# Kernel tuning notes

Measured on AMD Instinct MI355X. Metric: run time of the kernel, lower is better.

The kernel has to match this reference:

```python
import jax, jax.numpy as jnp
import numpy as np

WS = 7            # window size (Wh = Ww = 7)
N = WS * WS       # tokens per window = 49
C = 96            # dim
H = 3             # num_heads
HD = C // H       # head_dim = 32
SCALE = HD ** -0.5
B_ = 8192         # num_windows * batch


def _rel_pos_index():
    coords = np.stack(np.meshgrid(np.arange(WS), np.arange(WS), indexing='ij'))  # [2,WS,WS]
    cf = coords.reshape(2, -1)                      # [2,N]
    rel = (cf[:, :, None] - cf[:, None, :]).transpose(1, 2, 0).astype(np.int64)  # [N,N,2]
    rel[:, :, 0] += WS - 1
    rel[:, :, 1] += WS - 1
    rel[:, :, 0] *= 2 * WS - 1
    return rel.sum(-1)                              # [N,N] in [0, 169)

REL_IDX = jnp.asarray(_rel_pos_index())


def _dwconv(img, kern):
    # img: [B,Wh,Ww,C], kern: [3,3,1,C] depthwise
    return jax.lax.conv_general_dilated(
        img, kern, window_strides=(1, 1), padding='SAME',
        dimension_numbers=('NHWC', 'HWIO', 'NHWC'), feature_group_count=C)


def _l2norm(t, eps=1e-12):
    n = jnp.sqrt(jnp.sum(t * t, axis=-1, keepdims=True))
    return t / jnp.maximum(n, eps)


def _forward(x, rpb_table, wq, bq, wk, bk, wv, bv, w_ps, b_ps,
             wq_sp, wk_sp, w_pc, b_pc, conv1, conv2, w_proj, b_proj):
    B = x.shape[0]
    # ---- spatial branch (windowed MHSA with relative position bias) ----
    q = (x @ wq + bq).reshape(B, N, H, HD).transpose(0, 2, 1, 3)  # [B,H,N,HD]
    k = (x @ wk + bk).reshape(B, N, H, HD).transpose(0, 2, 1, 3)
    v_inp = x @ wv + bv                                            # [B,N,C]
    v = v_inp.reshape(B, N, H, HD).transpose(0, 2, 1, 3)
    attn = jnp.einsum('bhnd,bhmd->bhnm', q * SCALE, k)             # [B,H,N,N]
    rpb = rpb_table[REL_IDX.reshape(-1)].reshape(N, N, H).transpose(2, 0, 1)  # [H,N,N]
    attn = jax.nn.softmax(attn + rpb[None], axis=-1)
    sp = jnp.einsum('bhnm,bhmd->bhnd', attn, v).transpose(0, 2, 1, 3).reshape(B, N, C)
    spatial_x = sp @ w_ps + b_ps                                   # [B,N,C]
    # ---- spectral branch (L2-normalized channel attention) ----
    qs = (x @ wq_sp).reshape(B, N, H, HD).transpose(0, 2, 3, 1)    # [B,H,HD,N]
    ks = (x @ wk_sp).reshape(B, N, H, HD).transpose(0, 2, 3, 1)
    vs = v_inp.reshape(B, N, H, HD).transpose(0, 2, 3, 1)
    qs = _l2norm(qs)
    ks = _l2norm(ks)
    cattn = jax.nn.softmax(jnp.einsum('bhdn,bhen->bhde', ks, qs) * SCALE, axis=-1)  # [B,H,HD,HD]
    xc = jnp.einsum('bhde,bhen->bhdn', cattn, vs)                  # [B,H,HD,N]
    xc = xc.transpose(0, 3, 1, 2).reshape(B, N, C)                 # [B,N,C]
    out_c = (xc @ w_pc + b_pc).reshape(B, WS, WS, C)
    # depthwise-conv positional embedding on v_inp
    v_img = v_inp.reshape(B, WS, WS, C)
    out_p = _dwconv(jax.nn.gelu(_dwconv(v_img, conv1), approximate=False), conv2)
    spectral_x = (out_c + out_p).reshape(B, N, C)
    # ---- fuse ----
    return jnp.concatenate([spatial_x, spectral_x], axis=-1) @ w_proj + b_proj


def setup_inputs() -> dict:
    key = jax.random.key(0)
    ks = jax.random.split(key, 18)
    p = lambda i, shape: jax.random.normal(ks[i], shape, dtype=jnp.float32) * 0.02
    return {
        'x': jax.random.normal(ks[0], (B_, N, C), dtype=jnp.float32),
        'rpb_table': p(1, ((2 * WS - 1) ** 2, H)),
        'wq': p(2, (C, C)), 'bq': p(3, (C,)),
        'wk': p(4, (C, C)), 'bk': p(5, (C,)),
        'wv': p(6, (C, C)), 'bv': p(7, (C,)),
        'w_ps': p(8, (C, C)), 'b_ps': p(9, (C,)),
        'wq_sp': p(10, (C, C)), 'wk_sp': p(11, (C, C)),
        'w_pc': p(12, (C, C)), 'b_pc': p(13, (C,)),
        'conv1': p(14, (3, 3, 1, C)), 'conv2': p(15, (3, 3, 1, C)),
        'w_proj': p(16, (2 * C, C)), 'b_proj': p(17, (C,)),
    }


def reference(x, rpb_table, wq, bq, wk, bk, wv, bv, w_ps, b_ps,
              wq_sp, wk_sp, w_pc, b_pc, conv1, conv2, w_proj, b_proj):
    return _forward(x, rpb_table, wq, bq, wk, bk, wv, bv, w_ps, b_ps,
                    wq_sp, wk_sp, w_pc, b_pc, conv1, conv2, w_proj, b_proj)
```

## Files before the change

### kernel.cpp

```cpp
#include <hip/hip_runtime.h>

#define NTOK 49
#define CDIM 96
#define NH   3
#define HD   32

typedef __bf16 bf16x8 __attribute__((ext_vector_type(8)));
typedef float f32x4 __attribute__((ext_vector_type(4)));

__device__ __forceinline__ unsigned short f2bf(float f) {
  union { float f; unsigned u; } v; v.f = f;
  unsigned r = v.u + 0x7FFFu + ((v.u >> 16) & 1u);
  return (unsigned short)(r >> 16);
}
__device__ __forceinline__ float bf2f(unsigned short h) {
  union { unsigned u; float f; } v; v.u = ((unsigned)h) << 16;
  return v.f;
}

__global__ void prep_weights(const float* __restrict__ wq,
                             const float* __restrict__ wk,
                             const float* __restrict__ wv,
                             const float* __restrict__ wq_sp,
                             const float* __restrict__ wk_sp,
                             const float* __restrict__ w_ps,
                             const float* __restrict__ b_ps,
                             const float* __restrict__ w_pc,
                             const float* __restrict__ b_pc,
                             const float* __restrict__ w_proj,
                             const float* __restrict__ b_proj,
                             unsigned short* __restrict__ wsS,
                             float* __restrict__ wsB)
{
  const int g0 = blockIdx.x * blockDim.x + threadIdx.x;
  const int gs = gridDim.x * blockDim.x;
  const int TOT = 73728 + 96;
  for (int idx = g0; idx < TOT; idx += gs) {
    if (idx < 27648) {
      int o = idx / 96, i = idx % 96;
      float v;
      if (o < 96)       v = wq_sp[i*96 + o];
      else if (o < 192) v = wk_sp[i*96 + (o-96)];
      else              v = wv  [i*96 + (o-192)];
      wsS[idx] = f2bf(v);
    } else if (idx < 46080) {
      int j = idx - 27648, o = j / 96, i = j % 96;
      int h = o >> 6, cc = o & 63;
      wsS[idx] = f2bf((cc < 32) ? wq[i*96 + h*32 + cc] : wk[i*96 + h*32 + (cc-32)]);
    } else if (idx < 55296) {
      int j = idx - 46080, o = j / 96, i = j % 96;
      float a = 0.f;
      for (int k = 0; k < 96; ++k) a += w_ps[i*96+k] * w_proj[k*96+o];
      wsS[idx] = f2bf(a);
    } else if (idx < 64512) {
      int j = idx - 55296, o = j / 96, i = j % 96;
      float a = 0.f;
      for (int k = 0; k < 96; ++k) a += w_pc[i*96+k] * w_proj[(96+k)*96+o];
      wsS[idx] = f2bf(a);
    } else if (idx < 73728) {
      int j = idx - 64512, o = j / 96, i = j % 96;
      wsS[idx] = f2bf(w_proj[(96+i)*96 + o]);
    } else {
      int o = idx - 73728;
      float a = b_proj[o];
      for (int k = 0; k < 96; ++k) {
        a += b_ps[k] * w_proj[k*96+o];
        a += b_pc[k] * w_proj[(96+k)*96+o];
      }
      wsB[o] = a;
    }
  }
}

__global__ __launch_bounds__(256, 3) void winattn_mfma3(
    const float* __restrict__ x,
    const float* __restrict__ rpb,
    const float* __restrict__ bq,
    const float* __restrict__ bk,
    const float* __restrict__ bv,
    const float* __restrict__ conv1w,
    const float* __restrict__ conv2w,
    const unsigned short* __restrict__ wcat1,
    const unsigned short* __restrict__ wcat2,
    const unsigned short* __restrict__ w1b,
    const unsigned short* __restrict__ w2b,
    const unsigned short* __restrict__ wpb,
    const float* __restrict__ bias_all,
    float* __restrict__ out)
{
  __shared__ __align__(16) unsigned short sm[26864];
  const int tid = threadIdx.x;
  const int blk = blockIdx.x;
  enum { X_O = 0, V_O = 4704, QS_O = 9408, KS_O = 14216,
         K_O = 19024, SC_O = 23728 };
  const float SCALE = 0.17677669529663687f;

  const int w  = tid >> 6;
  const int l  = tid & 63;
  const int lr = l & 15;
  const int lg = l >> 4;
  float* const rn = (float*)&sm[K_O];

  {
    const float* xg = x + (size_t)blk * 4704;
    for (int i = tid; i < 1176; i += 256) {
      const float4 v = *(const float4*)&xg[i*4];
      union { unsigned short s[4]; uint2 u; } p;
      p.s[0] = f2bf(v.x); p.s[1] = f2bf(v.y); p.s[2] = f2bf(v.z); p.s[3] = f2bf(v.w);
      *(uint2*)&sm[X_O + i*4] = p.u;
    }
  }
  __syncthreads();

  {
    const int xrow = X_O + (16*w + lr)*96 + lg*8;
    const bf16x8 a0 = *(const bf16x8*)&sm[xrow];
    const bf16x8 a1 = *(const bf16x8*)&sm[xrow + 32];
    const bf16x8 a2 = *(const bf16x8*)&sm[xrow + 64];
    for (int t = 0; t < 18; ++t) {
      const int c = 16*t + lr;
      const bf16x8 b0 = *(const bf16x8*)&wcat1[c*96 + lg*8];
      const bf16x8 b1 = *(const bf16x8*)&wcat1[c*96 + 32 + lg*8];
      const bf16x8 b2 = *(const bf16x8*)&wcat1[c*96 + 64 + lg*8];
      f32x4 acc = {0.f, 0.f, 0.f, 0.f};
      acc = __builtin_amdgcn_mfma_f32_16x16x32_bf16(a0, b0, acc, 0, 0, 0);
      acc = __builtin_amdgcn_mfma_f32_16x16x32_bf16(a1, b1, acc, 0, 0, 0);
      acc = __builtin_amdgcn_mfma_f32_16x16x32_bf16(a2, b2, acc, 0, 0, 0);
      int base, col, strd; float bias = 0.f;
      if (t < 6)       { base = QS_O; col = c;       strd = 98; }
      else if (t < 12) { base = KS_O; col = c - 96;  strd = 98; }
      else             { base = V_O;  col = c - 192; strd = 96; bias = bv[c-192]; }
      #pragma unroll
      for (int r = 0; r < 4; ++r) {
        const int tok = 16*w + lg*4 + r;
        if (tok < NTOK) sm[base + tok*strd + col] = f2bf(acc[r] + bias);
      }
    }
  }
  __syncthreads();

  if (tid < 192) {
    const int c    = (tid < 96) ? tid : tid - 96;
    const int base = (tid < 96) ? QS_O : KS_O;
    float ss = 0.f;
    for (int n = 0; n < NTOK; ++n) { const float v = bf2f(sm[base + n*98 + c]); ss += v*v; }
    rn[tid] = 1.0f / fmaxf(sqrtf(ss), 1e-12f);
  }
  __syncthreads();

  {
    for (int jb = 0; jb < 3; ++jb) {
      const int job = w*3 + jb, rt = job >> 1, ct = job & 1, h = rt >> 1;
      const int qc = h*32 + 16*ct + lr;
      union { unsigned short u[8]; bf16x8 v; } a0u, a1u, b0u, b1u;
      #pragma unroll
      for (int j = 0; j < 8; ++j) {
        const int k0 = lg*8 + j, k1 = 32 + k0;
        a0u.u[j] = sm[KS_O + k0*98 + 16*rt + lr];
        b0u.u[j] = sm[QS_O + k0*98 + qc];
        a1u.u[j] = (k1 < NTOK) ? sm[KS_O + k1*98 + 16*rt + lr] : (unsigned short)0;
        b1u.u[j] = (k1 < NTOK) ? sm[QS_O + k1*98 + qc] : (unsigned short)0;
      }
      f32x4 acc = {0.f, 0.f, 0.f, 0.f};
      acc = __builtin_amdgcn_mfma_f32_16x16x32_bf16(a0u.v, b0u.v, acc, 0, 0, 0);
      acc = __builtin_amdgcn_mfma_f32_16x16x32_bf16(a1u.v, b1u.v, acc, 0, 0, 0);
      const float rq = rn[qc];
      #pragma unroll
      for (int r = 0; r < 4; ++r) {
        const int dq = 16*rt + lg*4 + r;
        sm[SC_O + dq*32 + 16*ct + lr] = f2bf(acc[r] * rq * rn[96 + dq] * SCALE);
      }
    }
  }
  __syncthreads();

  {
    const int xrow = X_O + (16*w + lr)*96 + lg*8;
    const bf16x8 a0 = *(const bf16x8*)&sm[xrow];
    const bf16x8 a1 = *(const bf16x8*)&sm[xrow + 32];
    const bf16x8 a2 = *(const bf16x8*)&sm[xrow + 64];
    for (int t = 0; t < 12; ++t) {
      const int c = 16*t + lr;
      const bf16x8 b0 = *(const bf16x8*)&wcat2[c*96 + lg*8];
      const bf16x8 b1 = *(const bf16x8*)&wcat2[c*96 + 32 + lg*8];
      const bf16x8 b2 = *(const bf16x8*)&wcat2[c*96 + 64 + lg*8];
      f32x4 acc = {0.f, 0.f, 0.f, 0.f};
      acc = __builtin_amdgcn_mfma_f32_16x16x32_bf16(a0, b0, acc, 0, 0, 0);
      acc = __builtin_amdgcn_mfma_f32_16x16x32_bf16(a1, b1, acc, 0, 0, 0);
      acc = __builtin_amdgcn_mfma_f32_16x16x32_bf16(a2, b2, acc, 0, 0, 0);
      const int h = t >> 2;
      const bool isq = (t & 3) < 2;
      const int cc = (t & 1)*16 + lr;
      const float bias = isq ? bq[h*32 + cc] : bk[h*32 + cc];
      const int dst = (isq ? X_O : K_O) + h*32 + cc;
      #pragma unroll
      for (int r = 0; r < 4; ++r) {
        const int tok = 16*w + lg*4 + r;
        if (tok < NTOK) sm[dst + tok*96] = f2bf(acc[r] + bias);
      }
    }
  }
  if (tid < 96) {
    const int base = SC_O + tid*32;
    const int off = (tid * 5) & 31;
    float m = -1e30f;
    for (int jj = 0; jj < 32; ++jj) { const int j = (jj + off) & 31;
      m = fmaxf(m, bf2f(sm[base + j])); }
    float s = 0.f;
    for (int jj = 0; jj < 32; ++jj) { const int j = (jj + off) & 31;
      s += __expf(bf2f(sm[base + j]) - m); }
    const float inv = 1.0f / s;
    for (int jj = 0; jj < 32; ++jj) { const int j = (jj + off) & 31;
      sm[base + j] = f2bf(__expf(bf2f(sm[base + j]) - m) * inv); }
  }
  __syncthreads();

  {
    for (int ctile = 0; ctile < 6; ++ctile) {
      const int h = ctile >> 1;
      const bf16x8 av  = *(const bf16x8*)&sm[V_O + (16*w + lr)*96 + h*32 + lg*8];
      const bf16x8 bc  = *(const bf16x8*)&sm[SC_O + (16*ctile + lr)*32 + lg*8];
      f32x4 acc = {0.f, 0.f, 0.f, 0.f};
      acc = __builtin_amdgcn_mfma_f32_16x16x32_bf16(av, bc, acc, 0, 0, 0);
      #pragma unroll
      for (int r = 0; r < 4; ++r) {
        const int tok = 16*w + lg*4 + r;
        if (tok < NTOK) sm[QS_O + tok*96 + 16*ctile + lr] = f2bf(acc[r]);
      }
    }
  }
  for (int idx = tid; idx < 588; idx += 256) {
    const int n = idx / 12, c0 = (idx % 12) * 8;
    const int y = n / 7, xx = n % 7;
    float a[8];
    #pragma unroll
    for (int j = 0; j < 8; ++j) a[j] = 0.f;
    #pragma unroll
    for (int dy = -1; dy <= 1; ++dy) {
      const int yy = y + dy;
      if (yy < 0 || yy >= 7) continue;
      #pragma unroll
      for (int dx = -1; dx <= 1; ++dx) {
        const int x2 = xx + dx;
        if (x2 < 0 || x2 >= 7) continue;
        union { bf16x8 v; unsigned short u[8]; } iv;
        iv.v = *(const bf16x8*)&sm[V_O + (yy*7 + x2)*96 + c0];
        const float* wp = conv1w + ((dy+1)*3 + (dx+1))*96 + c0;
        #pragma unroll
        for (int j = 0; j < 8; ++j) a[j] += bf2f(iv.u[j]) * wp[j];
      }
    }
    union { unsigned short u[8]; bf16x8 v; } ov;
    #pragma unroll
    for (int j = 0; j < 8; ++j) {
      const float g = a[j];
      ov.u[j] = f2bf(0.5f * g * (1.0f + erff(g * 0.70710678118654752f)));
    }
    *(bf16x8*)&sm[KS_O + n*96 + c0] = ov.v;
  }
  __syncthreads();

  float hov[3][8];
  {
    #pragma unroll
    for (int it = 0; it < 3; ++it) {
      const int e = tid + it*256;
      #pragma unroll
      for (int j = 0; j < 8; ++j) hov[it][j] = 0.f;
      if (e < 588) {
        const int n = e / 12, c0 = (e % 12) * 8;
        const int y = n / 7, xx = n % 7;
        #pragma unroll
        for (int dy = -1; dy <= 1; ++dy) {
          const int yy = y + dy;
          if (yy < 0 || yy >= 7) continue;
          #pragma unroll
          for (int dx = -1; dx <= 1; ++dx) {
            const int x2 = xx + dx;
            if (x2 < 0 || x2 >= 7) continue;
            union { bf16x8 v; unsigned short u[8]; } iv;
            iv.v = *(const bf16x8*)&sm[KS_O + (yy*7 + x2)*96 + c0];
            const float* wp = conv2w + ((dy+1)*3 + (dx+1))*96 + c0;
            #pragma unroll
            for (int j = 0; j < 8; ++j) hov[it][j] += bf2f(iv.u[j]) * wp[j];
          }
        }
      }
    }
    for (int zi = tid; zi < 735; zi += 256)
      sm[SC_O + (zi/15)*64 + 49 + zi%15] = 0;
  }
  __syncthreads();
  {
    #pragma unroll
    for (int it = 0; it < 3; ++it) {
      const int e = tid + it*256;
      if (e < 588) {
        const int n = e / 12, c0 = (e % 12) * 8;
        union { unsigned short u[8]; bf16x8 v; } ov;
        #pragma unroll
        for (int j = 0; j < 8; ++j) ov.u[j] = f2bf(hov[it][j]);
        *(bf16x8*)&sm[KS_O + n*96 + c0] = ov.v;
      }
    }
  }
  __syncthreads();

  for (int h = 0; h < NH; ++h) {
    {
      const bf16x8 aq = *(const bf16x8*)&sm[X_O + (16*w + lr)*96 + h*32 + lg*8];
      #pragma unroll
      for (int nt = 0; nt < 4; ++nt) {
        const bf16x8 bk8 = *(const bf16x8*)&sm[K_O + (16*nt + lr)*96 + h*32 + lg*8];
        f32x4 acc = {0.f, 0.f, 0.f, 0.f};
        acc = __builtin_amdgcn_mfma_f32_16x16x32_bf16(aq, bk8, acc, 0, 0, 0);
        #pragma unroll
        for (int r = 0; r < 4; ++r) {
          const int row = 16*w + lg*4 + r;
          const int col = 16*nt + lr;
          if (row < NTOK && col < NTOK) {
            const int ridx = (row/7 - col/7 + 6)*13 + (row%7 - col%7 + 6);
            sm[SC_O + row*64 + col] = f2bf(acc[r] * SCALE + rpb[ridx*NH + h]);
          }
        }
      }
    }
    __syncthreads();
    if (tid < 196) {
      const int row = tid >> 2, p = tid & 3;
      const int cS = p * 13;
      const int cnt = (p == 3) ? 10 : 13;
      const int ro = row % cnt;
      const int base = SC_O + row*64 + cS;
      float m = -1e30f;
      for (int i = 0; i < cnt; ++i) {
        int j = i + ro; if (j >= cnt) j -= cnt;
        m = fmaxf(m, bf2f(sm[base + j]));
      }
      m = fmaxf(m, __shfl_xor(m, 1, 4));
      m = fmaxf(m, __shfl_xor(m, 2, 4));
      float s = 0.f;
      for (int i = 0; i < cnt; ++i) {
        int j = i + ro; if (j >= cnt) j -= cnt;
        s += __expf(bf2f(sm[base + j]) - m);
      }
      s += __shfl_xor(s, 1, 4);
      s += __shfl_xor(s, 2, 4);
      const float inv = 1.0f / s;
      for (int i = 0; i < cnt; ++i) {
        int j = i + ro; if (j >= cnt) j -= cnt;
        sm[base + j] = f2bf(__expf(bf2f(sm[base + j]) - m) * inv);
      }
    }
    __syncthreads();
    {
      const int prow = (16*w + lr < 48) ? (16*w + lr) : 48;
      const bf16x8 ap0 = *(const bf16x8*)&sm[SC_O + prow*64 + lg*8];
      const bf16x8 ap1 = *(const bf16x8*)&sm[SC_O + prow*64 + 32 + lg*8];
      #pragma unroll
      for (int nt = 0; nt < 2; ++nt) {
        f32x4 acc = {0.f, 0.f, 0.f, 0.f};
        union { unsigned short u[8]; bf16x8 v; } cv;
        #pragma unroll
        for (int j = 0; j < 8; ++j)
          cv.u[j] = sm[V_O + (lg*8 + j)*96 + h*32 + 16*nt + lr];
        acc = __builtin_amdgcn_mfma_f32_16x16x32_bf16(ap0, cv.v, acc, 0, 0, 0);
        #pragma unroll
        for (int j = 0; j < 8; ++j)
          cv.u[j] = sm[V_O + (32 + lg*8 + j)*96 + h*32 + 16*nt + lr];
        acc = __builtin_amdgcn_mfma_f32_16x16x32_bf16(ap1, cv.v, acc, 0, 0, 0);
        #pragma unroll
        for (int r = 0; r < 4; ++r) {
          const int tok = 16*w + lg*4 + r;
          if (tok < NTOK) sm[X_O + tok*96 + h*32 + 16*nt + lr] = f2bf(acc[r]);
        }
      }
    }
    __syncthreads();
  }

  {
    f32x4 acc[6];
    #pragma unroll
    for (int t = 0; t < 6; ++t) acc[t] = (f32x4){0.f, 0.f, 0.f, 0.f};
    const int Ao[3] = { X_O, QS_O, KS_O };
    const unsigned short* const Ws[3] = { w1b, w2b, wpb };
    #pragma unroll
    for (int s = 0; s < 3; ++s) {
      const int arow = Ao[s] + (16*w + lr)*96 + lg*8;
      const bf16x8 a0 = *(const bf16x8*)&sm[arow];
      const bf16x8 a1 = *(const bf16x8*)&sm[arow + 32];
      const bf16x8 a2 = *(const bf16x8*)&sm[arow + 64];
      #pragma unroll
      for (int t = 0; t < 6; ++t) {
        const int o = 16*t + lr;
        const bf16x8 b0 = *(const bf16x8*)&Ws[s][o*96 + lg*8];
        const bf16x8 b1 = *(const bf16x8*)&Ws[s][o*96 + 32 + lg*8];
        const bf16x8 b2 = *(const bf16x8*)&Ws[s][o*96 + 64 + lg*8];
        acc[t] = __builtin_amdgcn_mfma_f32_16x16x32_bf16(a0, b0, acc[t], 0, 0, 0);
        acc[t] = __builtin_amdgcn_mfma_f32_16x16x32_bf16(a1, b1, acc[t], 0, 0, 0);
        acc[t] = __builtin_amdgcn_mfma_f32_16x16x32_bf16(a2, b2, acc[t], 0, 0, 0);
      }
    }
    float* og = out + (size_t)blk * 4704;
    #pragma unroll
    for (int t = 0; t < 6; ++t) {
      const int co = 16*t + lr;
      const float bb = bias_all[co];
      #pragma unroll
      for (int r = 0; r < 4; ++r) {
        const int tok = 16*w + lg*4 + r;
        if (tok < NTOK) og[tok*96 + co] = acc[t][r] + bb;
      }
    }
  }
}

extern "C" void kernel_launch(void* const* d_in, const int* in_sizes, int n_in,
                              void* d_out, int out_size, void* d_ws, size_t ws_size,
                              hipStream_t stream)
{
  const float* x      = (const float*)d_in[0];
  const float* rpbt   = (const float*)d_in[1];
  const float* wq     = (const float*)d_in[2];
  const float* bq     = (const float*)d_in[3];
  const float* wk     = (const float*)d_in[4];
  const float* bk     = (const float*)d_in[5];
  const float* wv     = (const float*)d_in[6];
  const float* bv     = (const float*)d_in[7];
  const float* w_ps   = (const float*)d_in[8];
  const float* b_ps   = (const float*)d_in[9];
  const float* wq_sp  = (const float*)d_in[10];
  const float* wk_sp  = (const float*)d_in[11];
  const float* w_pc   = (const float*)d_in[12];
  const float* b_pc   = (const float*)d_in[13];
  const float* conv1  = (const float*)d_in[14];
  const float* conv2  = (const float*)d_in[15];
  const float* w_proj = (const float*)d_in[16];
  const float* b_proj = (const float*)d_in[17];

  unsigned short* wsS = (unsigned short*)d_ws;
  float* wsB = (float*)((char*)d_ws + (size_t)2*73728);

  prep_weights<<<80, 256, 0, stream>>>(wq, wk, wv, wq_sp, wk_sp, w_ps, b_ps,
                                       w_pc, b_pc, w_proj, b_proj, wsS, wsB);

  const int nblk = in_sizes[0] / (NTOK*CDIM);
  winattn_mfma3<<<nblk, 256, 0, stream>>>(x, rpbt, bq, bk, bv, conv1, conv2,
      wsS, wsS + 27648, wsS + 46080, wsS + 55296, wsS + 64512, wsB,
      (float*)d_out);
}
```

Measured before the change: 871.3 us.

## Merge projection GEMMs, transpose spectral Q/K, precompute RPB, double-buffer head scores

Merges the two input projection MFMA loops into a single 30-tile pass, removing one barrier. Spectral Q/K are stored transposed with vectorized L2 normalization applied in place. The relative position bias is expanded once into a padded table in the prep kernel, and f2bf now uses a native bf16 cast. Per-head attention alternates between two score buffers so one head's PV overlaps the next head's QK^T, which cuts barriers but adds LDS use and layout complexity.

```diff
diff --git a/kernel.cpp b/kernel.cpp
--- a/kernel.cpp
+++ b/kernel.cpp
@@ -4,18 +4,17 @@
 #define CDIM 96
 #define NH   3
 #define HD   32
+#define TS   52
 
 typedef __bf16 bf16x8 __attribute__((ext_vector_type(8)));
 typedef float f32x4 __attribute__((ext_vector_type(4)));
-
-__device__ __forceinline__ unsigned short f2bf(float f) {
-  union { float f; unsigned u; } v; v.f = f;
-  unsigned r = v.u + 0x7FFFu + ((v.u >> 16) & 1u);
-  return (unsigned short)(r >> 16);
+typedef unsigned short u16;
+
+__device__ __forceinline__ u16 f2bf(float f) {
+  union { __bf16 h; u16 u; } v; v.h = (__bf16)f; return v.u;
 }
-__device__ __forceinline__ float bf2f(unsigned short h) {
-  union { unsigned u; float f; } v; v.u = ((unsigned)h) << 16;
-  return v.f;
+__device__ __forceinline__ float bf2f(u16 h) {
+  union { unsigned u; float f; } v; v.u = ((unsigned)h) << 16; return v.f;
 }
 
 __global__ void prep_weights(const float* __restrict__ wq,
@@ -29,12 +28,13 @@
                              const float* __restrict__ b_pc,
                              const float* __restrict__ w_proj,
                              const float* __restrict__ b_proj,
+                             const float* __restrict__ rpb,
                              unsigned short* __restrict__ wsS,
                              float* __restrict__ wsB)
 {
   const int g0 = blockIdx.x * blockDim.x + threadIdx.x;
   const int gs = gridDim.x * blockDim.x;
-  const int TOT = 73728 + 96;
+  const int TOT = 73728 + 96 + 3*49*64;
   for (int idx = g0; idx < TOT; idx += gs) {
     if (idx < 27648) {
       int o = idx / 96, i = idx % 96;
@@ -60,7 +60,7 @@
     } else if (idx < 73728) {
       int j = idx - 64512, o = j / 96, i = j % 96;
       wsS[idx] = f2bf(w_proj[(96+i)*96 + o]);
-    } else {
+    } else if (idx < 73824) {
       int o = idx - 73728;
       float a = b_proj[o];
       for (int k = 0; k < 96; ++k) {
@@ -68,13 +68,21 @@
         a += b_pc[k] * w_proj[(96+k)*96+o];
       }
       wsB[o] = a;
+    } else {
+      int j = idx - 73824;
+      int h = j / 3136, rr = (j % 3136) / 64, cc = j % 64;
+      float v = 0.f;
+      if (cc < NTOK) {
+        const int ridx = (rr/7 - cc/7 + 6)*13 + (rr%7 - cc%7 + 6);
+        v = rpb[ridx*NH + h];
+      }
+      wsB[96 + j] = v;
     }
   }
 }
 
-__global__ __launch_bounds__(256, 3) void winattn_mfma3(
+__global__ __launch_bounds__(256, 3) void winattn_v4(
     const float* __restrict__ x,
-    const float* __restrict__ rpb,
     const float* __restrict__ bq,
     const float* __restrict__ bk,
     const float* __restrict__ bv,
@@ -86,26 +94,26 @@
     const unsigned short* __restrict__ w2b,
     const unsigned short* __restrict__ wpb,
     const float* __restrict__ bias_all,
+    const float* __restrict__ rpbf,
     float* __restrict__ out)
 {
-  __shared__ __align__(16) unsigned short sm[26864];
+  __shared__ __align__(16) u16 sm[27232];
   const int tid = threadIdx.x;
   const int blk = blockIdx.x;
-  enum { X_O = 0, V_O = 4704, QS_O = 9408, KS_O = 14216,
-         K_O = 19024, SC_O = 23728 };
+  enum { X_O = 0, V_O = 4704, QT_O = 9408, KT_O = 14400,
+         K_O = 19392, SC_O = 24096 };
   const float SCALE = 0.17677669529663687f;
 
   const int w  = tid >> 6;
   const int l  = tid & 63;
   const int lr = l & 15;
   const int lg = l >> 4;
-  float* const rn = (float*)&sm[K_O];
 
   {
     const float* xg = x + (size_t)blk * 4704;
     for (int i = tid; i < 1176; i += 256) {
       const float4 v = *(const float4*)&xg[i*4];
-      union { unsigned short s[4]; uint2 u; } p;
+      union { u16 s[4]; uint2 u; } p;
       p.s[0] = f2bf(v.x); p.s[1] = f2bf(v.y); p.s[2] = f2bf(v.z); p.s[3] = f2bf(v.w);
       *(uint2*)&sm[X_O + i*4] = p.u;
     }
@@ -117,89 +125,105 @@
     const bf16x8 a0 = *(const bf16x8*)&sm[xrow];
     const bf16x8 a1 = *(const bf16x8*)&sm[xrow + 32];
     const bf16x8 a2 = *(const bf16x8*)&sm[xrow + 64];
-    for (int t = 0; t < 18; ++t) {
-      const int c = 16*t + lr;
-      const bf16x8 b0 = *(const bf16x8*)&wcat1[c*96 + lg*8];
-      const bf16x8 b1 = *(const bf16x8*)&wcat1[c*96 + 32 + lg*8];
-      const bf16x8 b2 = *(const bf16x8*)&wcat1[c*96 + 64 + lg*8];
+    const int t0 = 16*w + 4*lg;
+    for (int t = 0; t < 30; ++t) {
+      const u16* wsrc = (t < 18) ? &wcat1[(16*t + lr)*96]
+                                 : &wcat2[(16*(t-18) + lr)*96];
+      const bf16x8 b0 = *(const bf16x8*)&wsrc[lg*8];
+      const bf16x8 b1 = *(const bf16x8*)&wsrc[32 + lg*8];
+      const bf16x8 b2 = *(const bf16x8*)&wsrc[64 + lg*8];
       f32x4 acc = {0.f, 0.f, 0.f, 0.f};
       acc = __builtin_amdgcn_mfma_f32_16x16x32_bf16(a0, b0, acc, 0, 0, 0);
       acc = __builtin_amdgcn_mfma_f32_16x16x32_bf16(a1, b1, acc, 0, 0, 0);
       acc = __builtin_amdgcn_mfma_f32_16x16x32_bf16(a2, b2, acc, 0, 0, 0);
-      int base, col, strd; float bias = 0.f;
-      if (t < 6)       { base = QS_O; col = c;       strd = 98; }
-      else if (t < 12) { base = KS_O; col = c - 96;  strd = 98; }
-      else             { base = V_O;  col = c - 192; strd = 96; bias = bv[c-192]; }
-      #pragma unroll
-      for (int r = 0; r < 4; ++r) {
-        const int tok = 16*w + lg*4 + r;
-        if (tok < NTOK) sm[base + tok*strd + col] = f2bf(acc[r] + bias);
+      if (t < 12) {
+        const int base = (t < 6) ? (QT_O + (16*t + lr)*TS)
+                                 : (KT_O + (16*(t-6) + lr)*TS);
+        u16 s0 = f2bf(acc[0]), s1 = f2bf(acc[1]), s2 = f2bf(acc[2]), s3 = f2bf(acc[3]);
+        if (t0 <= 44) {
+          uint2 pk; pk.x = (unsigned)s0 | ((unsigned)s1 << 16);
+          pk.y = (unsigned)s2 | ((unsigned)s3 << 16);
+          *(uint2*)&sm[base + t0] = pk;
+        } else if (t0 == 48) {
+          uint2 pk; pk.x = (unsigned)s0; pk.y = 0u;
+          *(uint2*)&sm[base + 48] = pk;
+        }
+      } else if (t < 18) {
+        const int c = 16*t + lr - 192;
+        const float bias = bv[c];
+        #pragma unroll
+        for (int r = 0; r < 4; ++r) {
+          const int tok = t0 + r;
+          if (tok < NTOK) sm[V_O + tok*96 + c] = f2bf(acc[r] + bias);
+        }
+      } else {
+        const int u = t - 18, h = u >> 2;
+        const bool isq = (u & 3) < 2;
+        const int cc = (u & 1)*16 + lr;
+        const float bias = isq ? bq[h*32 + cc] : bk[h*32 + cc];
+        const int dst = (isq ? X_O : K_O) + h*32 + cc;
+        #pragma unroll
+        for (int r = 0; r < 4; ++r) {
+          const int tok = t0 + r;
+          if (tok < NTOK) sm[dst + tok*96] = f2bf(acc[r] + bias);
+        }
       }
     }
   }
   __syncthreads();
 
   if (tid < 192) {
-    const int c    = (tid < 96) ? tid : tid - 96;
-    const int base = (tid < 96) ? QS_O : KS_O;
+    const int base = (tid < 96) ? (QT_O + tid*TS) : (KT_O + (tid-96)*TS);
     float ss = 0.f;
-    for (int n = 0; n < NTOK; ++n) { const float v = bf2f(sm[base + n*98 + c]); ss += v*v; }
-    rn[tid] = 1.0f / fmaxf(sqrtf(ss), 1e-12f);
+    #pragma unroll
+    for (int i = 0; i < 12; ++i) {
+      const uint2 uu = *(const uint2*)&sm[base + i*4];
+      const float v0 = bf2f((u16)(uu.x & 0xFFFF)), v1 = bf2f((u16)(uu.x >> 16));
+      const float v2 = bf2f((u16)(uu.y & 0xFFFF)), v3 = bf2f((u16)(uu.y >> 16));
+      ss += v0*v0 + v1*v1 + v2*v2 + v3*v3;
+    }
+    { const float v = bf2f(sm[base + 48]); ss += v*v; }
+    const float rn = 1.0f / fmaxf(sqrtf(ss), 1e-12f);
+    #pragma unroll
+    for (int i = 0; i < 12; ++i) {
+      uint2 uu = *(const uint2*)&sm[base + i*4];
+      const u16 o0 = f2bf(bf2f((u16)(uu.x & 0xFFFF)) * rn);
+      const u16 o1 = f2bf(bf2f((u16)(uu.x >> 16)) * rn);
+      const u16 o2 = f2bf(bf2f((u16)(uu.y & 0xFFFF)) * rn);
+      const u16 o3 = f2bf(bf2f((u16)(uu.y >> 16)) * rn);
+      uu.x = (unsigned)o0 | ((unsigned)o1 << 16);
+      uu.y = (unsigned)o2 | ((unsigned)o3 << 16);
+      *(uint2*)&sm[base + i*4] = uu;
+    }
+    sm[base + 48] = f2bf(bf2f(sm[base + 48]) * rn);
   }
   __syncthreads();
 
   {
+    union U8 { uint2 q[2]; bf16x8 v; };
     for (int jb = 0; jb < 3; ++jb) {
       const int job = w*3 + jb, rt = job >> 1, ct = job & 1, h = rt >> 1;
-      const int qc = h*32 + 16*ct + lr;
-      union { unsigned short u[8]; bf16x8 v; } a0u, a1u, b0u, b1u;
-      #pragma unroll
-      for (int j = 0; j < 8; ++j) {
-        const int k0 = lg*8 + j, k1 = 32 + k0;
-        a0u.u[j] = sm[KS_O + k0*98 + 16*rt + lr];
-        b0u.u[j] = sm[QS_O + k0*98 + qc];
-        a1u.u[j] = (k1 < NTOK) ? sm[KS_O + k1*98 + 16*rt + lr] : (unsigned short)0;
-        b1u.u[j] = (k1 < NTOK) ? sm[QS_O + k1*98 + qc] : (unsigned short)0;
-      }
+      const int abase = KT_O + (16*rt + lr)*TS + lg*8;
+      const int bbase = QT_O + (h*32 + 16*ct + lr)*TS + lg*8;
+      U8 A0, B0, A1, B1;
+      A0.q[0] = *(const uint2*)&sm[abase];      A0.q[1] = *(const uint2*)&sm[abase + 4];
+      B0.q[0] = *(const uint2*)&sm[bbase];      B0.q[1] = *(const uint2*)&sm[bbase + 4];
+      A1.q[0] = *(const uint2*)&sm[abase + 32]; A1.q[1] = *(const uint2*)&sm[abase + 36];
+      B1.q[0] = *(const uint2*)&sm[bbase + 32]; B1.q[1] = *(const uint2*)&sm[bbase + 36];
+      if (lg == 2)      { A1.q[0].x &= 0xFFFFu; A1.q[0].y = 0u; A1.q[1].x = 0u; A1.q[1].y = 0u; }
+      else if (lg == 3) { A1.q[0].x = 0u; A1.q[0].y = 0u; A1.q[1].x = 0u; A1.q[1].y = 0u; }
       f32x4 acc = {0.f, 0.f, 0.f, 0.f};
-      acc = __builtin_amdgcn_mfma_f32_16x16x32_bf16(a0u.v, b0u.v, acc, 0, 0, 0);
-      acc = __builtin_amdgcn_mfma_f32_16x16x32_bf16(a1u.v, b1u.v, acc, 0, 0, 0);
-      const float rq = rn[qc];
+      acc = __builtin_amdgcn_mfma_f32_16x16x32_bf16(A0.v, B0.v, acc, 0, 0, 0);
+      acc = __builtin_amdgcn_mfma_f32_16x16x32_bf16(A1.v, B1.v, acc, 0, 0, 0);
       #pragma unroll
       for (int r = 0; r < 4; ++r) {
         const int dq = 16*rt + lg*4 + r;
-        sm[SC_O + dq*32 + 16*ct + lr] = f2bf(acc[r] * rq * rn[96 + dq] * SCALE);
-      }
-    }
-  }
-  __syncthreads();
-
-  {
-    const int xrow = X_O + (16*w + lr)*96 + lg*8;
-    const bf16x8 a0 = *(const bf16x8*)&sm[xrow];
-    const bf16x8 a1 = *(const bf16x8*)&sm[xrow + 32];
-    const bf16x8 a2 = *(const bf16x8*)&sm[xrow + 64];
-    for (int t = 0; t < 12; ++t) {
-      const int c = 16*t + lr;
-      const bf16x8 b0 = *(const bf16x8*)&wcat2[c*96 + lg*8];
-      const bf16x8 b1 = *(const bf16x8*)&wcat2[c*96 + 32 + lg*8];
-      const bf16x8 b2 = *(const bf16x8*)&wcat2[c*96 + 64 + lg*8];
-      f32x4 acc = {0.f, 0.f, 0.f, 0.f};
-      acc = __builtin_amdgcn_mfma_f32_16x16x32_bf16(a0, b0, acc, 0, 0, 0);
-      acc = __builtin_amdgcn_mfma_f32_16x16x32_bf16(a1, b1, acc, 0, 0, 0);
-      acc = __builtin_amdgcn_mfma_f32_16x16x32_bf16(a2, b2, acc, 0, 0, 0);
-      const int h = t >> 2;
-      const bool isq = (t & 3) < 2;
-      const int cc = (t & 1)*16 + lr;
-      const float bias = isq ? bq[h*32 + cc] : bk[h*32 + cc];
-      const int dst = (isq ? X_O : K_O) + h*32 + cc;
-      #pragma unroll
-      for (int r = 0; r < 4; ++r) {
-        const int tok = 16*w + lg*4 + r;
-        if (tok < NTOK) sm[dst + tok*96] = f2bf(acc[r] + bias);
-      }
-    }
-  }
+        sm[SC_O + dq*32 + 16*ct + lr] = f2bf(acc[r] * SCALE);
+      }
+    }
+  }
+  __syncthreads();
+
   if (tid < 96) {
     const int base = SC_O + tid*32;
     const int off = (tid * 5) & 31;
@@ -213,125 +237,35 @@
     for (int jj = 0; jj < 32; ++jj) { const int j = (jj + off) & 31;
       sm[base + j] = f2bf(__expf(bf2f(sm[base + j]) - m) * inv); }
   }
-  __syncthreads();
-
-  {
-    for (int ctile = 0; ctile < 6; ++ctile) {
-      const int h = ctile >> 1;
-      const bf16x8 av  = *(const bf16x8*)&sm[V_O + (16*w + lr)*96 + h*32 + lg*8];
-      const bf16x8 bc  = *(const bf16x8*)&sm[SC_O + (16*ctile + lr)*32 + lg*8];
+  for (int zi = tid; zi < 735; zi += 256)
+    sm[KT_O + (zi/15)*64 + 49 + zi%15] = 0;
+  __syncthreads();
+
+  auto QKT = [&](int h, int scb) {
+    const bf16x8 aq = *(const bf16x8*)&sm[X_O + (16*w + lr)*96 + h*32 + lg*8];
+    #pragma unroll
+    for (int nt = 0; nt < 4; ++nt) {
+      const bf16x8 bk8 = *(const bf16x8*)&sm[K_O + (16*nt + lr)*96 + h*32 + lg*8];
       f32x4 acc = {0.f, 0.f, 0.f, 0.f};
-      acc = __builtin_amdgcn_mfma_f32_16x16x32_bf16(av, bc, acc, 0, 0, 0);
+      acc = __builtin_amdgcn_mfma_f32_16x16x32_bf16(aq, bk8, acc, 0, 0, 0);
+      const int col = 16*nt + lr;
       #pragma unroll
       for (int r = 0; r < 4; ++r) {
-        const int tok = 16*w + lg*4 + r;
-        if (tok < NTOK) sm[QS_O + tok*96 + 16*ctile + lr] = f2bf(acc[r]);
-      }
-    }
-  }
-  for (int idx = tid; idx < 588; idx += 256) {
-    const int n = idx / 12, c0 = (idx % 12) * 8;
-    const int y = n / 7, xx = n % 7;
-    float a[8];
-    #pragma unroll
-    for (int j = 0; j < 8; ++j) a[j] = 0.f;
-    #pragma unroll
-    for (int dy = -1; dy <= 1; ++dy) {
-      const int yy = y + dy;
-      if (yy < 0 || yy >= 7) continue;
-      #pragma unroll
-      for (int dx = -1; dx <= 1; ++dx) {
-        const int x2 = xx + dx;
-        if (x2 < 0 || x2 >= 7) continue;
-        union { bf16x8 v; unsigned short u[8]; } iv;
-        iv.v = *(const bf16x8*)&sm[V_O + (yy*7 + x2)*96 + c0];
-        const float* wp = conv1w + ((dy+1)*3 + (dx+1))*96 + c0;
-        #pragma unroll
-        for (int j = 0; j < 8; ++j) a[j] += bf2f(iv.u[j]) * wp[j];
-      }
-    }
-    union { unsigned short u[8]; bf16x8 v; } ov;
-    #pragma unroll
-    for (int j = 0; j < 8; ++j) {
-      const float g = a[j];
-      ov.u[j] = f2bf(0.5f * g * (1.0f + erff(g * 0.70710678118654752f)));
-    }
-    *(bf16x8*)&sm[KS_O + n*96 + c0] = ov.v;
-  }
-  __syncthreads();
-
-  float hov[3][8];
-  {
-    #pragma unroll
-    for (int it = 0; it < 3; ++it) {
-      const int e = tid + it*256;
-      #pragma unroll
-      for (int j = 0; j < 8; ++j) hov[it][j] = 0.f;
-      if (e < 588) {
-        const int n = e / 12, c0 = (e % 12) * 8;
-        const int y = n / 7, xx = n % 7;
-        #pragma unroll
-        for (int dy = -1; dy <= 1; ++dy) {
-          const int yy = y + dy;
-          if (yy < 0 || yy >= 7) continue;
-          #pragma unroll
-          for (int dx = -1; dx <= 1; ++dx) {
-            const int x2 = xx + dx;
-            if (x2 < 0 || x2 >= 7) continue;
-            union { bf16x8 v; unsigned short u[8]; } iv;
-            iv.v = *(const bf16x8*)&sm[KS_O + (yy*7 + x2)*96 + c0];
-            const float* wp = conv2w + ((dy+1)*3 + (dx+1))*96 + c0;
-            #pragma unroll
-            for (int j = 0; j < 8; ++j) hov[it][j] += bf2f(iv.u[j]) * wp[j];
-          }
-        }
-      }
-    }
-    for (int zi = tid; zi < 735; zi += 256)
-      sm[SC_O + (zi/15)*64 + 49 + zi%15] = 0;
-  }
-  __syncthreads();
-  {
-    #pragma unroll
-    for (int it = 0; it < 3; ++it) {
-      const int e = tid + it*256;
-      if (e < 588) {
-        const int n = e / 12, c0 = (e % 12) * 8;
-        union { unsigned short u[8]; bf16x8 v; } ov;
-        #pragma unroll
-        for (int j = 0; j < 8; ++j) ov.u[j] = f2bf(hov[it][j]);
-        *(bf16x8*)&sm[KS_O + n*96 + c0] = ov.v;
-      }
-    }
-  }
-  __syncthreads();
-
-  for (int h = 0; h < NH; ++h) {
-    {
-      const bf16x8 aq = *(const bf16x8*)&sm[X_O + (16*w + lr)*96 + h*32 + lg*8];
-      #pragma unroll
-      for (int nt = 0; nt < 4; ++nt) {
-        const bf16x8 bk8 = *(const bf16x8*)&sm[K_O + (16*nt + lr)*96 + h*32 + lg*8];
-        f32x4 acc = {0.f, 0.f, 0.f, 0.f};
-        acc = __builtin_amdgcn_mfma_f32_16x16x32_bf16(aq, bk8, acc, 0, 0, 0);
-        #pragma unroll
-        for (int r = 0; r < 4; ++r) {
-          const int row = 16*w + lg*4 + r;
-          const int col = 16*nt + lr;
-          if (row < NTOK && col < NTOK) {
-            const int ridx = (row/7 - col/7 + 6)*13 + (row%7 - col%7 + 6);
-            sm[SC_O + row*64 + col] = f2bf(acc[r] * SCALE + rpb[ridx*NH + h]);
-          }
-        }
-      }
-    }
-    __syncthreads();
+        const int row = 16*w + lg*4 + r;
+        const int rc = (row < 48) ? row : 48;
+        const float bias = rpbf[(h*49 + rc)*64 + col];
+        if (row < NTOK && col < NTOK)
+          sm[scb + row*64 + col] = f2bf(acc[r] * SCALE + bias);
+      }
+    }
+  };
+  auto SMAX = [&](int scb) {
     if (tid < 196) {
       const int row = tid >> 2, p = tid & 3;
       const int cS = p * 13;
       const int cnt = (p == 3) ? 10 : 13;
       const int ro = row % cnt;
-      const int base = SC_O + row*64 + cS;
+      const int base = scb + row*64 + cS;
       float m = -1e30f;
       for (int i = 0; i < cnt; ++i) {
         int j = i + ro; if (j >= cnt) j -= cnt;
@@ -352,39 +286,131 @@
         sm[base + j] = f2bf(__expf(bf2f(sm[base + j]) - m) * inv);
       }
     }
-    __syncthreads();
-    {
-      const int prow = (16*w + lr < 48) ? (16*w + lr) : 48;
-      const bf16x8 ap0 = *(const bf16x8*)&sm[SC_O + prow*64 + lg*8];
-      const bf16x8 ap1 = *(const bf16x8*)&sm[SC_O + prow*64 + 32 + lg*8];
-      #pragma unroll
-      for (int nt = 0; nt < 2; ++nt) {
-        f32x4 acc = {0.f, 0.f, 0.f, 0.f};
-        union { unsigned short u[8]; bf16x8 v; } cv;
+  };
+  auto PV = [&](int h, int scb) {
+    const int prow = (16*w + lr < 48) ? (16*w + lr) : 48;
+    const bf16x8 ap0 = *(const bf16x8*)&sm[scb + prow*64 + lg*8];
+    const bf16x8 ap1 = *(const bf16x8*)&sm[scb + prow*64 + 32 + lg*8];
+    #pragma unroll
+    for (int nt = 0; nt < 2; ++nt) {
+      f32x4 acc = {0.f, 0.f, 0.f, 0.f};
+      union { u16 u[8]; bf16x8 v; } cv;
+      #pragma unroll
+      for (int j = 0; j < 8; ++j)
+        cv.u[j] = sm[V_O + (lg*8 + j)*96 + h*32 + 16*nt + lr];
+      acc = __builtin_amdgcn_mfma_f32_16x16x32_bf16(ap0, cv.v, acc, 0, 0, 0);
+      #pragma unroll
+      for (int j = 0; j < 8; ++j)
+        cv.u[j] = sm[V_O + (32 + lg*8 + j)*96 + h*32 + 16*nt + lr];
+      acc = __builtin_amdgcn_mfma_f32_16x16x32_bf16(ap1, cv.v, acc, 0, 0, 0);
+      #pragma unroll
+      for (int r = 0; r < 4; ++r) {
+        const int tok = 16*w + lg*4 + r;
+        if (tok < NTOK) sm[X_O + tok*96 + h*32 + 16*nt + lr] = f2bf(acc[r]);
+      }
+    }
+  };
+
+  {
+    for (int ctile = 0; ctile < 6; ++ctile) {
+      const int h = ctile >> 1;
+      const bf16x8 av = *(const bf16x8*)&sm[V_O + (16*w + lr)*96 + h*32 + lg*8];
+      const bf16x8 bc = *(const bf16x8*)&sm[SC_O + (16*ctile + lr)*32 + lg*8];
+      f32x4 acc = {0.f, 0.f, 0.f, 0.f};
+      acc = __builtin_amdgcn_mfma_f32_16x16x32_bf16(av, bc, acc, 0, 0, 0);
+      #pragma unroll
+      for (int r = 0; r < 4; ++r) {
+        const int tok = 16*w + lg*4 + r;
+        if (tok < NTOK) sm[QT_O + tok*96 + 16*ctile + lr] = f2bf(acc[r]);
+      }
+    }
+    QKT(0, KT_O);
+  }
+  __syncthreads();
+
+  SMAX(KT_O);
+  if (tid >= 196) {
+    for (int zi = tid - 196; zi < 735; zi += 60)
+      sm[SC_O + (zi/15)*64 + 49 + zi%15] = 0;
+  }
+  __syncthreads();
+
+  PV(0, KT_O); QKT(1, SC_O);
+  __syncthreads();
+  SMAX(SC_O);
+  __syncthreads();
+  PV(1, SC_O); QKT(2, KT_O);
+  __syncthreads();
+  SMAX(KT_O);
+  __syncthreads();
+  PV(2, KT_O);
+  __syncthreads();
+
+  for (int idx = tid; idx < 588; idx += 256) {
+    const int n = idx / 12, c0 = (idx % 12) * 8;
+    const int y = n / 7, xx = n % 7;
+    float a[8];
+    #pragma unroll
+    for (int j = 0; j < 8; ++j) a[j] = 0.f;
+    #pragma unroll
+    for (int dy = -1; dy <= 1; ++dy) {
+      const int yy = y + dy;
+      if (yy < 0 || yy >= 7) continue;
+      #pragma unroll
+      for (int dx = -1; dx <= 1; ++dx) {
+        const int x2 = xx + dx;
+        if (x2 < 0 || x2 >= 7) continue;
+        union { bf16x8 v; u16 u[8]; } iv;
+        iv.v = *(const bf16x8*)&sm[V_O + (yy*7 + x2)*96 + c0];
+        const float* wp = conv1w + ((dy+1)*3 + (dx+1))*96 + c0;
         #pragma unroll
-        for (int j = 0; j < 8; ++j)
-          cv.u[j] = sm[V_O + (lg*8 + j)*96 + h*32 + 16*nt + lr];
-        acc = __builtin_amdgcn_mfma_f32_16x16x32_bf16(ap0, cv.v, acc, 0, 0, 0);
+        for (int j = 0; j < 8; ++j) a[j] += bf2f(iv.u[j]) * wp[j];
+      }
+    }
+    union { u16 u[8]; bf16x8 v; } ov;
+    #pragma unroll
+    for (int j = 0; j < 8; ++j) {
+      const float g = a[j];
+      ov.u[j] = f2bf(0.5f * g * (1.0f + erff(g * 0.70710678118654752f)));
+    }
+    *(bf16x8*)&sm[KT_O + n*96 + c0] = ov.v;
+  }
+  __syncthreads();
+
+  for (int idx = tid; idx < 588; idx += 256) {
+    const int n = idx / 12, c0 = (idx % 12) * 8;
+    const int y = n / 7, xx = n % 7;
+    float a[8];
+    #pragma unroll
+    for (int j = 0; j < 8; ++j) a[j] = 0.f;
+    #pragma unroll
+    for (int dy = -1; dy <= 1; ++dy) {
+      const int yy = y + dy;
+      if (yy < 0 || yy >= 7) continue;
+      #pragma unroll
+      for (int dx = -1; dx <= 1; ++dx) {
+        const int x2 = xx + dx;
+        if (x2 < 0 || x2 >= 7) continue;
+        union { bf16x8 v; u16 u[8]; } iv;
+        iv.v = *(const bf16x8*)&sm[KT_O + (yy*7 + x2)*96 + c0];
+        const float* wp = conv2w + ((dy+1)*3 + (dx+1))*96 + c0;
         #pragma unroll
-        for (int j = 0; j < 8; ++j)
-          cv.u[j] = sm[V_O + (32 + lg*8 + j)*96 + h*32 + 16*nt + lr];
-        acc = __builtin_amdgcn_mfma_f32_16x16x32_bf16(ap1, cv.v, acc, 0, 0, 0);
-        #pragma unroll
-        for (int r = 0; r < 4; ++r) {
-          const int tok = 16*w + lg*4 + r;
-          if (tok < NTOK) sm[X_O + tok*96 + h*32 + 16*nt + lr] = f2bf(acc[r]);
-        }
-      }
-    }
-    __syncthreads();
-  }
+        for (int j = 0; j < 8; ++j) a[j] += bf2f(iv.u[j]) * wp[j];
+      }
+    }
+    union { u16 u[8]; bf16x8 v; } ov;
+    #pragma unroll
+    for (int j = 0; j < 8; ++j) ov.u[j] = f2bf(a[j]);
+    *(bf16x8*)&sm[V_O + n*96 + c0] = ov.v;
+  }
+  __syncthreads();
 
   {
     f32x4 acc[6];
     #pragma unroll
     for (int t = 0; t < 6; ++t) acc[t] = (f32x4){0.f, 0.f, 0.f, 0.f};
-    const int Ao[3] = { X_O, QS_O, KS_O };
-    const unsigned short* const Ws[3] = { w1b, w2b, wpb };
+    const int Ao[3] = { X_O, QT_O, V_O };
+    const u16* const Ws[3] = { w1b, w2b, wpb };
     #pragma unroll
     for (int s = 0; s < 3; ++s) {
       const int arow = Ao[s] + (16*w + lr)*96 + lg*8;
@@ -443,10 +469,11 @@
   float* wsB = (float*)((char*)d_ws + (size_t)2*73728);
 
   prep_weights<<<80, 256, 0, stream>>>(wq, wk, wv, wq_sp, wk_sp, w_ps, b_ps,
-                                       w_pc, b_pc, w_proj, b_proj, wsS, wsB);
+                                       w_pc, b_pc, w_proj, b_proj, rpbt,
+                                       wsS, wsB);
 
   const int nblk = in_sizes[0] / (NTOK*CDIM);
-  winattn_mfma3<<<nblk, 256, 0, stream>>>(x, rpbt, bq, bk, bv, conv1, conv2,
-      wsS, wsS + 27648, wsS + 46080, wsS + 55296, wsS + 64512, wsB,
-      (float*)d_out);
+  winattn_v4<<<nblk, 256, 0, stream>>>(x, bq, bk, bv, conv1, conv2,
+      wsS, wsS + 27648, wsS + 46080, wsS + 55296, wsS + 64512,
+      wsB, wsB + 96, (float*)d_out);
 }
```

Result: slower. 1.003 ms (+15.1%).
